# Performance work log

Measured on AMD Instinct MI355X. Metric: run time of the kernel, lower is better.

## Reference

```python
import jax, jax.numpy as jnp
import numpy as np

HIDDEN_SIZE = 1024  # used for scaling, per the module's __init__
NEG_INF = -1e9

def setup_inputs() -> dict:
    key = jax.random.key(0)
    kq, kk, kv, km = jax.random.split(key, 4)
    B, H, S, D = 2, 16, 2048, 64
    query = jax.random.normal(kq, (B, H, S, D), dtype=jnp.float32)
    k_ = jax.random.normal(kk, (B, H, S, D), dtype=jnp.float32)
    v_ = jax.random.normal(kv, (B, H, S, D), dtype=jnp.float32)
    mask = jax.random.randint(km, (B, S), 0, 2, dtype=jnp.int32)
    return {"query": query, "key": k_, "value": v_, "mask": mask}

def reference(query, key, value, mask):
    # scores: [B,H,S,S]
    scores = jnp.einsum("bhqd,bhkd->bhqk", query, key)
    scores = scores / jnp.sqrt(jnp.float32(HIDDEN_SIZE))
    m = mask.astype(jnp.float32)[:, None, None, :]  # [B,1,1,S]
    scores = scores + NEG_INF * (1.0 - m)
    weights = jax.nn.softmax(scores, axis=-1)
    return jnp.einsum("bhqk,bhkd->bhqd", weights, value)
```

## Files before the change

### kernel.cpp

```cpp
#include <hip/hip_runtime.h>
#include <hip/hip_bf16.h>

typedef __bf16 bf16x8 __attribute__((ext_vector_type(8)));
typedef __bf16 bf16x4 __attribute__((ext_vector_type(4)));
typedef float  f32x4  __attribute__((ext_vector_type(4)));

typedef __attribute__((address_space(3))) void lds_void;
typedef __attribute__((address_space(1))) const void gbl_void;

constexpr int SEQ = 2048;
constexpr int HD  = 64;
constexpr int KT  = 64;
constexpr int QB  = 64;
constexpr int NT  = SEQ / KT;
constexpr int LDP = 72;

__global__ __launch_bounds__(256)
void prepass(const float* __restrict__ K, const float* __restrict__ V,
             __bf16* __restrict__ Kf, __bf16* __restrict__ Vf)
{
    __shared__ __bf16 Kt[64][72];
    __shared__ __bf16 Vt[64][72];

    const int t = blockIdx.x, bh = blockIdx.y, tid = threadIdx.x;
    const size_t base = (size_t)bh * SEQ * HD + (size_t)t * 64 * HD;

    #pragma unroll
    for (int p = 0; p < 4; ++p) {
        int idx = p * 256 + tid;
        int row = idx >> 4, c4 = (idx & 15) * 4;
        float4 kv = *(const float4*)(K + base + row * HD + c4);
        bf16x4 kb;
        kb[0]=(__bf16)kv.x; kb[1]=(__bf16)kv.y; kb[2]=(__bf16)kv.z; kb[3]=(__bf16)kv.w;
        *(bf16x4*)&Kt[row][c4] = kb;
        float4 vv = *(const float4*)(V + base + row * HD + c4);
        bf16x4 vb;
        vb[0]=(__bf16)vv.x; vb[1]=(__bf16)vv.y; vb[2]=(__bf16)vv.z; vb[3]=(__bf16)vv.w;
        *(bf16x4*)&Vt[row][c4] = vb;
    }
    __syncthreads();

    __bf16* kd = Kf + (size_t)(bh * NT + t) * 4096;
    __bf16* vd = Vf + (size_t)(bh * NT + t) * 4096;
    #pragma unroll
    for (int p = 0; p < 2; ++p) {
        int gran = p * 256 + tid;
        int frag = gran >> 6, l = gran & 63, lo = l & 15, hi = l >> 4;
        int s = frag >> 1, kh = frag & 1;
        bf16x8 ko = *(const bf16x8*)&Kt[s*16 + lo][kh*32 + hi*8];
        *(bf16x8*)(kd + gran * 8) = ko;
        bf16x8 vo;
        #pragma unroll
        for (int j = 0; j < 8; ++j)
            vo[j] = Vt[kh*32 + hi*8 + j][s*16 + lo];
        *(bf16x8*)(vd + gran * 8) = vo;
    }
}

__global__ __launch_bounds__(256, 3)
void attn_fwd4(const float* __restrict__ Q, const __bf16* __restrict__ Kf,
               const __bf16* __restrict__ Vf, const int* __restrict__ mask,
               float* __restrict__ out)
{
    __shared__ __bf16 Kl[2][4096];
    __shared__ __bf16 Vl[2][4096];
    __shared__ __bf16 Pl[4][16][LDP];
    __shared__ unsigned long long Ml[NT];

    const int tid = threadIdx.x;
    const int w   = tid >> 6;
    const int l   = tid & 63;
    const int lo  = l & 15;
    const int hi  = l >> 4;

    const int id   = blockIdx.x;
    const int virt = (id & 7) * 128 + (id >> 3);
    const int bh   = virt >> 5;
    const int qb   = virt & 31;
    const int b    = bh >> 4;
    const size_t base = (size_t)bh * SEQ * HD;
    const int qbase = qb * QB + w * 16;

    {
        const int4* mp = (const int4*)(mask + b * SEQ);
        int4 m0 = mp[tid * 2], m1 = mp[tid * 2 + 1];
        unsigned byte =
            ((unsigned)(m0.x != 0)     ) | ((unsigned)(m0.y != 0) << 1) |
            ((unsigned)(m0.z != 0) << 2) | ((unsigned)(m0.w != 0) << 3) |
            ((unsigned)(m1.x != 0) << 4) | ((unsigned)(m1.y != 0) << 5) |
            ((unsigned)(m1.z != 0) << 6) | ((unsigned)(m1.w != 0) << 7);
        ((unsigned char*)Ml)[tid] = (unsigned char)byte;
    }

    bf16x8 qf[2];
    {
        const float* qp = Q + base + (size_t)(qbase + lo) * HD;
        #pragma unroll
        for (int kh = 0; kh < 2; ++kh) {
            const float4 a = *(const float4*)(qp + kh*32 + hi*8);
            const float4 c = *(const float4*)(qp + kh*32 + hi*8 + 4);
            bf16x8 f;
            f[0]=(__bf16)a.x; f[1]=(__bf16)a.y; f[2]=(__bf16)a.z; f[3]=(__bf16)a.w;
            f[4]=(__bf16)c.x; f[5]=(__bf16)c.y; f[6]=(__bf16)c.z; f[7]=(__bf16)c.w;
            qf[kh] = f;
        }
    }

    const __bf16* Ksrc = Kf + (size_t)bh * NT * 4096;
    const __bf16* Vsrc = Vf + (size_t)bh * NT * 4096;

    auto stage = [&](int buf, int t) {
        const __bf16* kg = Ksrc + (size_t)t * 4096;
        const __bf16* vg = Vsrc + (size_t)t * 4096;
        #pragma unroll
        for (int r = 0; r < 2; ++r) {
            __builtin_amdgcn_global_load_lds(
                (gbl_void*)(kg + (size_t)(r*256 + tid) * 8),
                (lds_void*)(&Kl[buf][0] + (r*256 + w*64) * 8), 16, 0, 0);
            __builtin_amdgcn_global_load_lds(
                (gbl_void*)(vg + (size_t)(r*256 + tid) * 8),
                (lds_void*)(&Vl[buf][0] + (r*256 + w*64) * 8), 16, 0, 0);
        }
    };

    f32x4 acc[4] = {{0,0,0,0},{0,0,0,0},{0,0,0,0},{0,0,0,0}};
    float m_run  = -INFINITY;
    float l_part = 0.f;

    stage(0, 0);
    __syncthreads();

    for (int t = 0; t < NT; ++t) {
        const int buf = t & 1;
        if (t + 1 < NT) stage(buf ^ 1, t + 1);

        float sv[4][4];
        const unsigned long long mb = Ml[t];
        __builtin_amdgcn_s_setprio(1);
        #pragma unroll
        for (int s = 0; s < 4; ++s) {
            bf16x8 k0 = *(const bf16x8*)&Kl[buf][(s*2+0) * 512 + l*8];
            bf16x8 k1 = *(const bf16x8*)&Kl[buf][(s*2+1) * 512 + l*8];
            f32x4 c = {0,0,0,0};
            c = __builtin_amdgcn_mfma_f32_16x16x32_bf16(k0, qf[0], c, 0, 0, 0);
            c = __builtin_amdgcn_mfma_f32_16x16x32_bf16(k1, qf[1], c, 0, 0, 0);
            const unsigned ms = (unsigned)(mb >> (s * 16));
            #pragma unroll
            for (int r = 0; r < 4; ++r)
                sv[s][r] = c[r] * 0.03125f +
                           (((ms >> (hi*4 + r)) & 1u) ? 0.f : -1e9f);
        }
        __builtin_amdgcn_s_setprio(0);

        bf16x8 vfr[8];
        #pragma unroll
        for (int f = 0; f < 8; ++f)
            vfr[f] = *(const bf16x8*)&Vl[buf][f * 512 + l*8];

        float pm = sv[0][0];
        #pragma unroll
        for (int s = 0; s < 4; ++s)
            #pragma unroll
            for (int r = 0; r < 4; ++r)
                pm = fmaxf(pm, sv[s][r]);

        if (!__all(pm - m_run <= 8.0f)) {
            float pmr = pm;
            pmr = fmaxf(pmr, __shfl_xor(pmr, 16));
            pmr = fmaxf(pmr, __shfl_xor(pmr, 32));
            const float mn  = fmaxf(m_run, pmr);
            const float scl = __expf(m_run - mn);
            m_run = mn;
            l_part *= scl;
            #pragma unroll
            for (int nt = 0; nt < 4; ++nt)
                #pragma unroll
                for (int r = 0; r < 4; ++r)
                    acc[nt][r] *= scl;
        }

        float p[4][4], ls = 0.f;
        #pragma unroll
        for (int s = 0; s < 4; ++s) {
            #pragma unroll
            for (int r = 0; r < 4; ++r) {
                p[s][r] = __expf(sv[s][r] - m_run);
                ls += p[s][r];
            }
        }
        l_part += ls;

        #pragma unroll
        for (int s = 0; s < 4; ++s) {
            bf16x4 pk;
            pk[0]=(__bf16)p[s][0]; pk[1]=(__bf16)p[s][1];
            pk[2]=(__bf16)p[s][2]; pk[3]=(__bf16)p[s][3];
            *(bf16x4*)&Pl[w][lo][s*16 + hi*4] = pk;
        }

        bf16x8 pa0 = *(const bf16x8*)&Pl[w][lo][hi * 8];
        bf16x8 pa1 = *(const bf16x8*)&Pl[w][lo][32 + hi * 8];
        __builtin_amdgcn_s_setprio(1);
        #pragma unroll
        for (int nt = 0; nt < 4; ++nt) {
            acc[nt] = __builtin_amdgcn_mfma_f32_16x16x32_bf16(vfr[nt*2+0], pa0, acc[nt], 0, 0, 0);
            acc[nt] = __builtin_amdgcn_mfma_f32_16x16x32_bf16(vfr[nt*2+1], pa1, acc[nt], 0, 0, 0);
        }
        __builtin_amdgcn_s_setprio(0);

        __syncthreads();
    }

    float lr = l_part;
    lr += __shfl_xor(lr, 16);
    lr += __shfl_xor(lr, 32);
    const float inv = 1.0f / lr;

    float* op = out + base + (size_t)(qbase + lo) * HD;
    #pragma unroll
    for (int nt = 0; nt < 4; ++nt)
        #pragma unroll
        for (int r = 0; r < 4; ++r)
            op[nt*16 + hi*4 + r] = acc[nt][r] * inv;
}

__global__ __launch_bounds__(256)
void attn_fwd_legacy(const float* __restrict__ Q, const float* __restrict__ K,
                     const float* __restrict__ V, const int* __restrict__ mask,
                     float* __restrict__ out)
{
    __shared__ __bf16 Kl[KT][LDP];
    __shared__ __bf16 Vl[HD][LDP];
    __shared__ __bf16 Pl[4][16][LDP];

    const int tid = threadIdx.x;
    const int w   = tid >> 6;
    const int l   = tid & 63;
    const int lo  = l & 15;
    const int hi  = l >> 4;

    const int bh = blockIdx.y;
    const int b  = bh >> 4;
    const size_t base = (size_t)bh * SEQ * HD;
    const int qbase = blockIdx.x * QB + w * 16;

    bf16x8 qf[2];
    {
        const float* qp = Q + base + (size_t)(qbase + lo) * HD;
        #pragma unroll
        for (int kh = 0; kh < 2; ++kh) {
            const float4 a = *(const float4*)(qp + kh*32 + hi*8);
            const float4 c = *(const float4*)(qp + kh*32 + hi*8 + 4);
            bf16x8 f;
            f[0]=(__bf16)a.x; f[1]=(__bf16)a.y; f[2]=(__bf16)a.z; f[3]=(__bf16)a.w;
            f[4]=(__bf16)c.x; f[5]=(__bf16)c.y; f[6]=(__bf16)c.z; f[7]=(__bf16)c.w;
            qf[kh] = f;
        }
    }

    f32x4 acc[4] = {{0,0,0,0},{0,0,0,0},{0,0,0,0},{0,0,0,0}};
    float m_run[4], l_run[4];
    #pragma unroll
    for (int r = 0; r < 4; ++r) { m_run[r] = -INFINITY; l_run[r] = 0.f; }

    const int* maskp = mask + b * SEQ;

    for (int k0 = 0; k0 < SEQ; k0 += KT) {
        #pragma unroll
        for (int i = 0; i < 4; ++i) {
            int e4 = i * 256 + tid;
            int key = e4 >> 4, d4 = (e4 & 15) * 4;
            float4 kv = *(const float4*)(K + base + (size_t)(k0 + key) * HD + d4);
            bf16x4 kb;
            kb[0]=(__bf16)kv.x; kb[1]=(__bf16)kv.y; kb[2]=(__bf16)kv.z; kb[3]=(__bf16)kv.w;
            *(bf16x4*)&Kl[key][d4] = kb;
        }
        #pragma unroll
        for (int i = 0; i < 4; ++i) {
            int e4 = i * 256 + tid;
            int key = e4 >> 4, d4 = (e4 & 15) * 4;
            float4 vv = *(const float4*)(V + base + (size_t)(k0 + key) * HD + d4);
            Vl[d4+0][key] = (__bf16)vv.x;
            Vl[d4+1][key] = (__bf16)vv.y;
            Vl[d4+2][key] = (__bf16)vv.z;
            Vl[d4+3][key] = (__bf16)vv.w;
        }
        __syncthreads();

        float sv[4][4];
        #pragma unroll
        for (int s = 0; s < 4; ++s) {
            f32x4 c = {0,0,0,0};
            bf16x8 kf0 = *(const bf16x8*)&Kl[s*16 + lo][hi*8];
            bf16x8 kf1 = *(const bf16x8*)&Kl[s*16 + lo][32 + hi*8];
            c = __builtin_amdgcn_mfma_f32_16x16x32_bf16(qf[0], kf0, c, 0, 0, 0);
            c = __builtin_amdgcn_mfma_f32_16x16x32_bf16(qf[1], kf1, c, 0, 0, 0);
            const int km = maskp[k0 + s*16 + lo];
            #pragma unroll
            for (int r = 0; r < 4; ++r)
                sv[s][r] = km ? (c[r] * 0.03125f) : -1e9f;
        }

        float tm[4];
        #pragma unroll
        for (int r = 0; r < 4; ++r)
            tm[r] = fmaxf(fmaxf(sv[0][r], sv[1][r]), fmaxf(sv[2][r], sv[3][r]));
        #pragma unroll
        for (int off = 1; off < 16; off <<= 1)
            #pragma unroll
            for (int r = 0; r < 4; ++r)
                tm[r] = fmaxf(tm[r], __shfl_xor(tm[r], off));

        float scl[4];
        #pragma unroll
        for (int r = 0; r < 4; ++r) {
            float mn = fmaxf(m_run[r], tm[r]);
            scl[r] = __expf(m_run[r] - mn);
            m_run[r] = mn;
        }
        float pv_[4][4], rs[4] = {0.f, 0.f, 0.f, 0.f};
        #pragma unroll
        for (int s = 0; s < 4; ++s)
            #pragma unroll
            for (int r = 0; r < 4; ++r) {
                float p = __expf(sv[s][r] - m_run[r]);
                pv_[s][r] = p;
                rs[r] += p;
            }
        #pragma unroll
        for (int off = 1; off < 16; off <<= 1)
            #pragma unroll
            for (int r = 0; r < 4; ++r)
                rs[r] += __shfl_xor(rs[r], off);
        #pragma unroll
        for (int r = 0; r < 4; ++r)
            l_run[r] = l_run[r] * scl[r] + rs[r];
        #pragma unroll
        for (int nt = 0; nt < 4; ++nt)
            #pragma unroll
            for (int r = 0; r < 4; ++r)
                acc[nt][r] *= scl[r];

        #pragma unroll
        for (int s = 0; s < 4; ++s)
            #pragma unroll
            for (int r = 0; r < 4; ++r)
                Pl[w][hi*4 + r][s*16 + lo] = (__bf16)pv_[s][r];

        bf16x8 pa0 = *(const bf16x8*)&Pl[w][lo][hi*8];
        bf16x8 pa1 = *(const bf16x8*)&Pl[w][lo][32 + hi*8];
        #pragma unroll
        for (int nt = 0; nt < 4; ++nt) {
            bf16x8 v0 = *(const bf16x8*)&Vl[nt*16 + lo][hi*8];
            bf16x8 v1 = *(const bf16x8*)&Vl[nt*16 + lo][32 + hi*8];
            acc[nt] = __builtin_amdgcn_mfma_f32_16x16x32_bf16(pa0, v0, acc[nt], 0, 0, 0);
            acc[nt] = __builtin_amdgcn_mfma_f32_16x16x32_bf16(pa1, v1, acc[nt], 0, 0, 0);
        }
        __syncthreads();
    }

    float inv[4];
    #pragma unroll
    for (int r = 0; r < 4; ++r) inv[r] = 1.0f / l_run[r];
    float* op = out + base + (size_t)qbase * HD;
    #pragma unroll
    for (int nt = 0; nt < 4; ++nt)
        #pragma unroll
        for (int r = 0; r < 4; ++r)
            op[(size_t)(hi*4 + r) * HD + nt*16 + lo] = acc[nt][r] * inv[r];
}

extern "C" void kernel_launch(void* const* d_in, const int* in_sizes, int n_in,
                              void* d_out, int out_size, void* d_ws, size_t ws_size,
                              hipStream_t stream) {
    (void)in_sizes; (void)n_in; (void)out_size;
    const float* Q  = (const float*)d_in[0];
    const float* K  = (const float*)d_in[1];
    const float* V  = (const float*)d_in[2];
    const int* mask = (const int*)d_in[3];
    float* out      = (float*)d_out;

    const size_t kv_elems = (size_t)32 * SEQ * HD;
    const size_t need = kv_elems * 2  * 2 ;

    if (ws_size >= need) {
        __bf16* Kf = (__bf16*)d_ws;
        __bf16* Vf = Kf + kv_elems;
        hipLaunchKernelGGL(prepass, dim3(NT, 32), dim3(256), 0, stream, K, V, Kf, Vf);
        hipLaunchKernelGGL(attn_fwd4, dim3(1024), dim3(256), 0, stream,
                           Q, Kf, Vf, mask, out);
    } else {
        hipLaunchKernelGGL(attn_fwd_legacy, dim3(SEQ / QB, 32), dim3(256), 0, stream,
                           Q, K, V, mask, out);
    }
}
```

Before: 165.2 us.

## Fold mask into V and row sums into MFMA, drop LDS P round-trip

Masked V rows are zeroed in the prepass, and the row sum is computed by an extra MFMA against a bf16 mask vector, so masked keys drop out of numerator and denominator without adding -1e9 to scores. K rows are permuted so the score accumulator layout matches the P operand layout, which removes the LDS store/load of P. The softmax scale is folded into Q, and occupancy is raised to 4 blocks per SU. The running max now includes masked scores, which could in principle underflow exp for unmasked keys, and the row sum is accumulated from bf16-rounded probabilities.

```diff
diff --git a/kernel.cpp b/kernel.cpp
--- a/kernel.cpp
+++ b/kernel.cpp
@@ -14,16 +14,20 @@
 constexpr int QB  = 64;
 constexpr int NT  = SEQ / KT;
 constexpr int LDP = 72;
+constexpr float QSCL = 0.03125f;
 
 __global__ __launch_bounds__(256)
 void prepass(const float* __restrict__ K, const float* __restrict__ V,
+             const int* __restrict__ mask,
              __bf16* __restrict__ Kf, __bf16* __restrict__ Vf)
 {
     __shared__ __bf16 Kt[64][72];
     __shared__ __bf16 Vt[64][72];
 
     const int t = blockIdx.x, bh = blockIdx.y, tid = threadIdx.x;
+    const int b = bh >> 4;
     const size_t base = (size_t)bh * SEQ * HD + (size_t)t * 64 * HD;
+    const int* maskp = mask + b * SEQ + t * 64;
 
     #pragma unroll
     for (int p = 0; p < 4; ++p) {
@@ -33,9 +37,11 @@
         bf16x4 kb;
         kb[0]=(__bf16)kv.x; kb[1]=(__bf16)kv.y; kb[2]=(__bf16)kv.z; kb[3]=(__bf16)kv.w;
         *(bf16x4*)&Kt[row][c4] = kb;
+        const float m01 = maskp[row] ? 1.0f : 0.0f;
         float4 vv = *(const float4*)(V + base + row * HD + c4);
         bf16x4 vb;
-        vb[0]=(__bf16)vv.x; vb[1]=(__bf16)vv.y; vb[2]=(__bf16)vv.z; vb[3]=(__bf16)vv.w;
+        vb[0]=(__bf16)(vv.x*m01); vb[1]=(__bf16)(vv.y*m01);
+        vb[2]=(__bf16)(vv.z*m01); vb[3]=(__bf16)(vv.w*m01);
         *(bf16x4*)&Vt[row][c4] = vb;
     }
     __syncthreads();
@@ -47,7 +53,8 @@
         int gran = p * 256 + tid;
         int frag = gran >> 6, l = gran & 63, lo = l & 15, hi = l >> 4;
         int s = frag >> 1, kh = frag & 1;
-        bf16x8 ko = *(const bf16x8*)&Kt[s*16 + lo][kh*32 + hi*8];
+        int krow = 32*(s>>1) + 8*(lo>>2) + 4*(s&1) + (lo&3);
+        bf16x8 ko = *(const bf16x8*)&Kt[krow][kh*32 + hi*8];
         *(bf16x8*)(kd + gran * 8) = ko;
         bf16x8 vo;
         #pragma unroll
@@ -57,15 +64,14 @@
     }
 }
 
-__global__ __launch_bounds__(256, 3)
-void attn_fwd4(const float* __restrict__ Q, const __bf16* __restrict__ Kf,
+__global__ __launch_bounds__(256, 4)
+void attn_fwd5(const float* __restrict__ Q, const __bf16* __restrict__ Kf,
                const __bf16* __restrict__ Vf, const int* __restrict__ mask,
                float* __restrict__ out)
 {
     __shared__ __bf16 Kl[2][4096];
     __shared__ __bf16 Vl[2][4096];
-    __shared__ __bf16 Pl[4][16][LDP];
-    __shared__ unsigned long long Ml[NT];
+    __shared__ __attribute__((aligned(16))) __bf16 Ml16[SEQ];
 
     const int tid = threadIdx.x;
     const int w   = tid >> 6;
@@ -84,12 +90,12 @@
     {
         const int4* mp = (const int4*)(mask + b * SEQ);
         int4 m0 = mp[tid * 2], m1 = mp[tid * 2 + 1];
-        unsigned byte =
-            ((unsigned)(m0.x != 0)     ) | ((unsigned)(m0.y != 0) << 1) |
-            ((unsigned)(m0.z != 0) << 2) | ((unsigned)(m0.w != 0) << 3) |
-            ((unsigned)(m1.x != 0) << 4) | ((unsigned)(m1.y != 0) << 5) |
-            ((unsigned)(m1.z != 0) << 6) | ((unsigned)(m1.w != 0) << 7);
-        ((unsigned char*)Ml)[tid] = (unsigned char)byte;
+        bf16x8 mm;
+        mm[0]=(__bf16)(m0.x?1.0f:0.0f); mm[1]=(__bf16)(m0.y?1.0f:0.0f);
+        mm[2]=(__bf16)(m0.z?1.0f:0.0f); mm[3]=(__bf16)(m0.w?1.0f:0.0f);
+        mm[4]=(__bf16)(m1.x?1.0f:0.0f); mm[5]=(__bf16)(m1.y?1.0f:0.0f);
+        mm[6]=(__bf16)(m1.z?1.0f:0.0f); mm[7]=(__bf16)(m1.w?1.0f:0.0f);
+        *(bf16x8*)&Ml16[tid * 8] = mm;
     }
 
     bf16x8 qf[2];
@@ -100,8 +106,10 @@
             const float4 a = *(const float4*)(qp + kh*32 + hi*8);
             const float4 c = *(const float4*)(qp + kh*32 + hi*8 + 4);
             bf16x8 f;
-            f[0]=(__bf16)a.x; f[1]=(__bf16)a.y; f[2]=(__bf16)a.z; f[3]=(__bf16)a.w;
-            f[4]=(__bf16)c.x; f[5]=(__bf16)c.y; f[6]=(__bf16)c.z; f[7]=(__bf16)c.w;
+            f[0]=(__bf16)(a.x*QSCL); f[1]=(__bf16)(a.y*QSCL);
+            f[2]=(__bf16)(a.z*QSCL); f[3]=(__bf16)(a.w*QSCL);
+            f[4]=(__bf16)(c.x*QSCL); f[5]=(__bf16)(c.y*QSCL);
+            f[6]=(__bf16)(c.z*QSCL); f[7]=(__bf16)(c.w*QSCL);
             qf[kh] = f;
         }
     }
@@ -124,8 +132,8 @@
     };
 
     f32x4 acc[4] = {{0,0,0,0},{0,0,0,0},{0,0,0,0},{0,0,0,0}};
+    f32x4 acc_l  = {0,0,0,0};
     float m_run  = -INFINITY;
-    float l_part = 0.f;
 
     stage(0, 0);
     __syncthreads();
@@ -134,8 +142,7 @@
         const int buf = t & 1;
         if (t + 1 < NT) stage(buf ^ 1, t + 1);
 
-        float sv[4][4];
-        const unsigned long long mb = Ml[t];
+        f32x4 sc[4];
         __builtin_amdgcn_s_setprio(1);
         #pragma unroll
         for (int s = 0; s < 4; ++s) {
@@ -144,11 +151,7 @@
             f32x4 c = {0,0,0,0};
             c = __builtin_amdgcn_mfma_f32_16x16x32_bf16(k0, qf[0], c, 0, 0, 0);
             c = __builtin_amdgcn_mfma_f32_16x16x32_bf16(k1, qf[1], c, 0, 0, 0);
-            const unsigned ms = (unsigned)(mb >> (s * 16));
-            #pragma unroll
-            for (int r = 0; r < 4; ++r)
-                sv[s][r] = c[r] * 0.03125f +
-                           (((ms >> (hi*4 + r)) & 1u) ? 0.f : -1e9f);
+            sc[s] = c;
         }
         __builtin_amdgcn_s_setprio(0);
 
@@ -156,13 +159,14 @@
         #pragma unroll
         for (int f = 0; f < 8; ++f)
             vfr[f] = *(const bf16x8*)&Vl[buf][f * 512 + l*8];
-
-        float pm = sv[0][0];
-        #pragma unroll
-        for (int s = 0; s < 4; ++s)
-            #pragma unroll
-            for (int r = 0; r < 4; ++r)
-                pm = fmaxf(pm, sv[s][r]);
+        bf16x8 am0 = *(const bf16x8*)&Ml16[t*64 + hi*8];
+        bf16x8 am1 = *(const bf16x8*)&Ml16[t*64 + 32 + hi*8];
+
+        float t0 = fmaxf(fmaxf(sc[0][0], sc[0][1]), fmaxf(sc[0][2], sc[0][3]));
+        float t1 = fmaxf(fmaxf(sc[1][0], sc[1][1]), fmaxf(sc[1][2], sc[1][3]));
+        float t2 = fmaxf(fmaxf(sc[2][0], sc[2][1]), fmaxf(sc[2][2], sc[2][3]));
+        float t3 = fmaxf(fmaxf(sc[3][0], sc[3][1]), fmaxf(sc[3][2], sc[3][3]));
+        float pm = fmaxf(fmaxf(t0, t1), fmaxf(t2, t3));
 
         if (!__all(pm - m_run <= 8.0f)) {
             float pmr = pm;
@@ -171,7 +175,7 @@
             const float mn  = fmaxf(m_run, pmr);
             const float scl = __expf(m_run - mn);
             m_run = mn;
-            l_part *= scl;
+            acc_l[0] *= scl;
             #pragma unroll
             for (int nt = 0; nt < 4; ++nt)
                 #pragma unroll
@@ -179,43 +183,31 @@
                     acc[nt][r] *= scl;
         }
 
-        float p[4][4], ls = 0.f;
+        bf16x8 pa0, pa1;
         #pragma unroll
         for (int s = 0; s < 4; ++s) {
             #pragma unroll
             for (int r = 0; r < 4; ++r) {
-                p[s][r] = __expf(sv[s][r] - m_run);
-                ls += p[s][r];
+                float pv = __expf(sc[s][r] - m_run);
+                if (s < 2) pa0[(s & 1) * 4 + r] = (__bf16)pv;
+                else       pa1[(s & 1) * 4 + r] = (__bf16)pv;
             }
         }
-        l_part += ls;
-
-        #pragma unroll
-        for (int s = 0; s < 4; ++s) {
-            bf16x4 pk;
-            pk[0]=(__bf16)p[s][0]; pk[1]=(__bf16)p[s][1];
-            pk[2]=(__bf16)p[s][2]; pk[3]=(__bf16)p[s][3];
-            *(bf16x4*)&Pl[w][lo][s*16 + hi*4] = pk;
-        }
-
-        bf16x8 pa0 = *(const bf16x8*)&Pl[w][lo][hi * 8];
-        bf16x8 pa1 = *(const bf16x8*)&Pl[w][lo][32 + hi * 8];
+
         __builtin_amdgcn_s_setprio(1);
         #pragma unroll
         for (int nt = 0; nt < 4; ++nt) {
             acc[nt] = __builtin_amdgcn_mfma_f32_16x16x32_bf16(vfr[nt*2+0], pa0, acc[nt], 0, 0, 0);
             acc[nt] = __builtin_amdgcn_mfma_f32_16x16x32_bf16(vfr[nt*2+1], pa1, acc[nt], 0, 0, 0);
         }
+        acc_l = __builtin_amdgcn_mfma_f32_16x16x32_bf16(am0, pa0, acc_l, 0, 0, 0);
+        acc_l = __builtin_amdgcn_mfma_f32_16x16x32_bf16(am1, pa1, acc_l, 0, 0, 0);
         __builtin_amdgcn_s_setprio(0);
 
         __syncthreads();
     }
 
-    float lr = l_part;
-    lr += __shfl_xor(lr, 16);
-    lr += __shfl_xor(lr, 32);
-    const float inv = 1.0f / lr;
-
+    const float inv = 1.0f / acc_l[0];
     float* op = out + base + (size_t)(qbase + lo) * HD;
     #pragma unroll
     for (int nt = 0; nt < 4; ++nt)
@@ -386,8 +378,9 @@
     if (ws_size >= need) {
         __bf16* Kf = (__bf16*)d_ws;
         __bf16* Vf = Kf + kv_elems;
-        hipLaunchKernelGGL(prepass, dim3(NT, 32), dim3(256), 0, stream, K, V, Kf, Vf);
-        hipLaunchKernelGGL(attn_fwd4, dim3(1024), dim3(256), 0, stream,
+        hipLaunchKernelGGL(prepass, dim3(NT, 32), dim3(256), 0, stream,
+                           K, V, mask, Kf, Vf);
+        hipLaunchKernelGGL(attn_fwd5, dim3(1024), dim3(256), 0, stream,
                            Q, Kf, Vf, mask, out);
     } else {
         hipLaunchKernelGGL(attn_fwd_legacy, dim3(SEQ / QB, 32), dim3(256), 0, stream,
```

New measurement: 144.1 us. 12.7% less time.
